# Performance work log

Hardware: AMD Instinct MI355X
Metric: run time of the kernel (lower is better)

Reference implementation:

```python
import jax, jax.numpy as jnp
import numpy as np

N_NODES = 100000
N_EDGES = 1600000
D_IN = 64


def _graph_conv(x, edge_src, edge_dst, W, b, n_nodes):
    # gather source features along edges, mean-aggregate at destinations,
    # then linear transform + ReLU (standard GraphConv semantics)
    msgs = x[edge_src]  # [E, d]
    agg = jax.ops.segment_sum(msgs, edge_dst, num_segments=n_nodes)  # [N, d]
    deg = jax.ops.segment_sum(jnp.ones((edge_src.shape[0],), x.dtype), edge_dst,
                              num_segments=n_nodes)  # [N]
    agg = agg / jnp.maximum(deg, 1.0)[:, None]
    return jax.nn.relu(agg @ W + b)


def setup_inputs() -> dict:
    key = jax.random.key(0)
    ks = jax.random.split(key, 6)
    node_features = jax.random.normal(ks[0], (N_NODES, D_IN), dtype=jnp.float32)
    edge_src = jax.random.randint(ks[1], (N_EDGES,), 0, N_NODES)
    edge_dst = jax.random.randint(ks[2], (N_EDGES,), 0, N_NODES)
    W1 = jax.random.normal(ks[3], (D_IN, 64), dtype=jnp.float32) * (1.0 / np.sqrt(D_IN))
    b1 = jnp.zeros((64,), jnp.float32)
    W2 = jax.random.normal(ks[4], (64, 32), dtype=jnp.float32) * (1.0 / np.sqrt(64))
    b2 = jnp.zeros((32,), jnp.float32)
    Wd = jax.random.normal(ks[5], (1, 1), dtype=jnp.float32)
    bd = jnp.zeros((1,), jnp.float32)
    return {"node_features": node_features, "edge_src": edge_src, "edge_dst": edge_dst,
            "W1": W1, "b1": b1, "W2": W2, "b2": b2, "Wd": Wd, "bd": bd}


def reference(node_features, edge_src, edge_dst, W1, b1, W2, b2, Wd, bd):
    n_nodes = node_features.shape[0]
    x = _graph_conv(node_features, edge_src, edge_dst, W1, b1, n_nodes)  # [N, 64]
    x = _graph_conv(x, edge_src, edge_dst, W2, b2, n_nodes)              # [N, 32]
    x = jnp.mean(x, axis=1, keepdims=True)                               # [N, 1]
    return jax.nn.sigmoid(x @ Wd + bd)                                   # [N, 1]
```

## Files before the change

### kernel.cpp

```cpp
#include <hip/hip_runtime.h>
#include <hip/hip_bf16.h>

#define N_NODES 100000
#define N_EDGES 1600000
#define N_PAD   100096
#define BSHIFT  10
#define NBUCKET 98
#define BCAP    19456
#define EPB     4096
#define NSCAT   391
#define NGEMM1  1563
#define PCAP    34816
#define ZROW    N_NODES

typedef float f32x2 __attribute__((ext_vector_type(2)));

__device__ __forceinline__ unsigned short f32_to_bf16(float f) {
    unsigned int u = __float_as_uint(f);
    unsigned int r = (u + 0x7fffu + ((u >> 16) & 1u)) >> 16;
    return (unsigned short)r;
}
__device__ __forceinline__ f32x2 up2(unsigned int p) {
    f32x2 r;
    r.x = __uint_as_float(p << 16);
    r.y = __uint_as_float(p & 0xffff0000u);
    return r;
}

__global__ void __launch_bounds__(256) k1_scatter_gemm64(
    const int* __restrict__ src, const int* __restrict__ dst,
    int* __restrict__ bcur, unsigned int* __restrict__ tmp,
    const float4* __restrict__ X4, const float* __restrict__ W,
    unsigned short* __restrict__ Y, int n_edges, int M) {
    extern __shared__ char smem[];
    int t = threadIdx.x;
    if (blockIdx.x < NSCAT) {
        int* lh = (int*)smem;
        int e0 = blockIdx.x * EPB;
        int ecnt = min(EPB, n_edges - e0);
        if (t < 128) lh[t] = 0;
        __syncthreads();
        const int4* s4 = (const int4*)(src + e0);
        const int4* d4 = (const int4*)(dst + e0);
        int4 sv[4], dv[4];
        #pragma unroll
        for (int j = 0; j < 4; j++) {
            int ib = t + j * 256;
            if (ib * 4 < ecnt) {
                sv[j] = s4[ib];
                dv[j] = d4[ib];
                atomicAdd(&lh[dv[j].x >> BSHIFT], 1);
                atomicAdd(&lh[dv[j].y >> BSHIFT], 1);
                atomicAdd(&lh[dv[j].z >> BSHIFT], 1);
                atomicAdd(&lh[dv[j].w >> BSHIFT], 1);
            }
        }
        __syncthreads();
        if (t < NBUCKET) {
            int c = lh[t];
            lh[t] = (c > 0) ? atomicAdd(&bcur[t], c) : 0;
        }
        __syncthreads();
        #pragma unroll
        for (int j = 0; j < 4; j++) {
            int ib = t + j * 256;
            if (ib * 4 < ecnt) {
                int ss[4] = {sv[j].x, sv[j].y, sv[j].z, sv[j].w};
                int dd[4] = {dv[j].x, dv[j].y, dv[j].z, dv[j].w};
                #pragma unroll
                for (int q = 0; q < 4; q++) {
                    int b = dd[q] >> BSHIFT;
                    int p = atomicAdd(&lh[b], 1);
                    if (p < BCAP)
                        tmp[(size_t)b * BCAP + p] =
                            ((unsigned)ss[q] << BSHIFT) | (unsigned)(dd[q] & 1023);
                }
            }
        }
        return;
    }
    float* sx = (float*)smem;
    float* sw = sx + 64 * 64;
    int base = (blockIdx.x - NSCAT) * 64;
    for (int i = t; i < 64 * 16; i += 256) {
        int r = i >> 4, c4 = i & 15;
        int row = base + r;
        float4 v = make_float4(0.f, 0.f, 0.f, 0.f);
        if (row < M) v = X4[(size_t)row * 16 + c4];
        int colp = (c4 * 4 + (r & 60)) & 63;
        *(float4*)&sx[r * 64 + colp] = v;
    }
    float4* sw4 = (float4*)sw;
    const float4* W4 = (const float4*)W;
    for (int i = t; i < 64 * 16; i += 256) sw4[i] = W4[i];
    __syncthreads();

    int tm = t & 15;
    int tn = t >> 4;
    int rbase = tm * 4;
    float acc[4][4] = {{0.f}};
    #pragma unroll 8
    for (int k = 0; k < 64; k++) {
        float4 b = sw4[k * 16 + tn];
        int kk = (k + rbase) & 63;
        float a0 = sx[(rbase + 0) * 64 + kk], a1 = sx[(rbase + 1) * 64 + kk];
        float a2 = sx[(rbase + 2) * 64 + kk], a3 = sx[(rbase + 3) * 64 + kk];
        acc[0][0] = fmaf(a0, b.x, acc[0][0]); acc[0][1] = fmaf(a0, b.y, acc[0][1]);
        acc[0][2] = fmaf(a0, b.z, acc[0][2]); acc[0][3] = fmaf(a0, b.w, acc[0][3]);
        acc[1][0] = fmaf(a1, b.x, acc[1][0]); acc[1][1] = fmaf(a1, b.y, acc[1][1]);
        acc[1][2] = fmaf(a1, b.z, acc[1][2]); acc[1][3] = fmaf(a1, b.w, acc[1][3]);
        acc[2][0] = fmaf(a2, b.x, acc[2][0]); acc[2][1] = fmaf(a2, b.y, acc[2][1]);
        acc[2][2] = fmaf(a2, b.z, acc[2][2]); acc[2][3] = fmaf(a2, b.w, acc[2][3]);
        acc[3][0] = fmaf(a3, b.x, acc[3][0]); acc[3][1] = fmaf(a3, b.y, acc[3][1]);
        acc[3][2] = fmaf(a3, b.z, acc[3][2]); acc[3][3] = fmaf(a3, b.w, acc[3][3]);
    }
    #pragma unroll
    for (int i = 0; i < 4; i++) {
        int row = base + rbase + i;
        if (row <= M) {
            ushort4 p;
            p.x = f32_to_bf16(acc[i][0]); p.y = f32_to_bf16(acc[i][1]);
            p.z = f32_to_bf16(acc[i][2]); p.w = f32_to_bf16(acc[i][3]);
            *(ushort4*)&Y[(size_t)row * 64 + tn * 4] = p;
        }
    }
}

__global__ void __launch_bounds__(1024) bucket_to_csr(
    const unsigned int* __restrict__ tmp, const int* __restrict__ bcur,
    int2* __restrict__ meta, int* __restrict__ col, int n_nodes) {
    __shared__ int nh[1024];
    __shared__ int wsum[16];
    int b = blockIdx.x;
    int t = threadIdx.x;
    int m = min(bcur[b], BCAP);
    const unsigned int* te = tmp + (size_t)b * BCAP;
    nh[t] = 0;
    __syncthreads();
    unsigned int rc[16];
    #pragma unroll
    for (int j = 0; j < 16; j++) {
        int i = t + j * 1024;
        if (i < m) {
            rc[j] = te[i];
            atomicAdd(&nh[rc[j] & 1023], 1);
        }
    }
    for (int i = t + 16384; i < m; i += 1024)
        atomicAdd(&nh[te[i] & 1023], 1);
    __syncthreads();
    int d  = nh[t];
    int pc = (d + 31) & ~31;
    int lane = t & 63;
    int incl = pc;
    #pragma unroll
    for (int o = 1; o < 64; o <<= 1) {
        int u = __shfl_up(incl, o);
        if (lane >= o) incl += u;
    }
    int w = t >> 6;
    if (lane == 63) wsum[w] = incl;
    __syncthreads();
    int woff = 0;
    #pragma unroll
    for (int q = 0; q < 16; q++) woff += (q < w) ? wsum[q] : 0;
    int begin = b * PCAP + woff + incl - pc;
    int node = (b << BSHIFT) + t;
    if (node < n_nodes) meta[node] = make_int2(begin, d);
    uint4 zz = make_uint4(ZROW, ZROW, ZROW, ZROW);
    uint4* cp = (uint4*)(col + begin);
    for (int q = 0; q < (pc >> 2); q++) cp[q] = zz;
    nh[t] = begin;
    __syncthreads();
    #pragma unroll
    for (int j = 0; j < 16; j++) {
        int i = t + j * 1024;
        if (i < m) {
            unsigned int e = rc[j];
            int pos = atomicAdd(&nh[e & 1023], 1);
            col[pos] = (int)(e >> BSHIFT);
        }
    }
    for (int i = t + 16384; i < m; i += 1024) {
        unsigned int e = te[i];
        int pos = atomicAdd(&nh[e & 1023], 1);
        col[pos] = (int)(e >> BSHIFT);
    }
}

__global__ void __launch_bounds__(256) gemm_n32(const float4* __restrict__ X4,
                                                const float* __restrict__ W,
                                                unsigned short* __restrict__ Z, int M) {
    __shared__ float sx[128][65];
    __shared__ float sw[64 * 32];
    int t = threadIdx.x;
    int base = blockIdx.x * 128;
    for (int i = t; i < 128 * 16; i += 256) {
        int r = i >> 4, c4 = i & 15;
        int row = base + r;
        float4 v = make_float4(0.f, 0.f, 0.f, 0.f);
        if (row < M) v = X4[(size_t)row * 16 + c4];
        sx[r][c4 * 4 + 0] = v.x; sx[r][c4 * 4 + 1] = v.y;
        sx[r][c4 * 4 + 2] = v.z; sx[r][c4 * 4 + 3] = v.w;
    }
    float4* sw4 = (float4*)sw;
    const float4* W4 = (const float4*)W;
    for (int i = t; i < 64 * 8; i += 256) sw4[i] = W4[i];
    __syncthreads();

    int tm = t & 31;
    int tn = t >> 5;
    float acc[4][4] = {{0.f}};
    #pragma unroll 8
    for (int k = 0; k < 64; k++) {
        float4 b = sw4[k * 8 + tn];
        float a0 = sx[tm * 4 + 0][k], a1 = sx[tm * 4 + 1][k];
        float a2 = sx[tm * 4 + 2][k], a3 = sx[tm * 4 + 3][k];
        acc[0][0] = fmaf(a0, b.x, acc[0][0]); acc[0][1] = fmaf(a0, b.y, acc[0][1]);
        acc[0][2] = fmaf(a0, b.z, acc[0][2]); acc[0][3] = fmaf(a0, b.w, acc[0][3]);
        acc[1][0] = fmaf(a1, b.x, acc[1][0]); acc[1][1] = fmaf(a1, b.y, acc[1][1]);
        acc[1][2] = fmaf(a1, b.z, acc[1][2]); acc[1][3] = fmaf(a1, b.w, acc[1][3]);
        acc[2][0] = fmaf(a2, b.x, acc[2][0]); acc[2][1] = fmaf(a2, b.y, acc[2][1]);
        acc[2][2] = fmaf(a2, b.z, acc[2][2]); acc[2][3] = fmaf(a2, b.w, acc[2][3]);
        acc[3][0] = fmaf(a3, b.x, acc[3][0]); acc[3][1] = fmaf(a3, b.y, acc[3][1]);
        acc[3][2] = fmaf(a3, b.z, acc[3][2]); acc[3][3] = fmaf(a3, b.w, acc[3][3]);
    }
    #pragma unroll
    for (int i = 0; i < 4; i++) {
        int row = base + tm * 4 + i;
        if (row <= M) {
            ushort4 p;
            p.x = f32_to_bf16(acc[i][0]); p.y = f32_to_bf16(acc[i][1]);
            p.z = f32_to_bf16(acc[i][2]); p.w = f32_to_bf16(acc[i][3]);
            *(ushort4*)&Z[(size_t)row * 32 + tn * 4] = p;
        }
    }
}

__global__ void __launch_bounds__(256) gather_relu64(
    const uint4* __restrict__ Y4, const int2* __restrict__ meta,
    const int* __restrict__ col, const float* __restrict__ b1,
    float4* __restrict__ H4, int n_nodes) {
    int n = blockIdx.x * 4 + (threadIdx.x >> 6);
    if (n >= n_nodes) return;
    int lane = threadIdx.x & 63;
    int g = lane >> 3;
    int c = lane & 7;
    int2 md = meta[n];
    int beg = md.x;
    int d = md.y;

    f32x2 acc[4];
    acc[0] = 0.f; acc[1] = 0.f; acc[2] = 0.f; acc[3] = 0.f;
    for (int i = 0; i < d; i += 32) {
        int s0 = col[beg + i + g];
        int s1 = col[beg + i + g + 8];
        int s2 = col[beg + i + g + 16];
        int s3 = col[beg + i + g + 24];
        uint4 v0 = Y4[(size_t)s0 * 8 + c];
        uint4 v1 = Y4[(size_t)s1 * 8 + c];
        uint4 v2 = Y4[(size_t)s2 * 8 + c];
        uint4 v3 = Y4[(size_t)s3 * 8 + c];
        acc[0] += (up2(v0.x) + up2(v1.x)) + (up2(v2.x) + up2(v3.x));
        acc[1] += (up2(v0.y) + up2(v1.y)) + (up2(v2.y) + up2(v3.y));
        acc[2] += (up2(v0.z) + up2(v1.z)) + (up2(v2.z) + up2(v3.z));
        acc[3] += (up2(v0.w) + up2(v1.w)) + (up2(v2.w) + up2(v3.w));
    }
    #pragma unroll
    for (int m = 8; m <= 32; m <<= 1) {
        #pragma unroll
        for (int q = 0; q < 4; q++) {
            acc[q].x += __shfl_xor(acc[q].x, m);
            acc[q].y += __shfl_xor(acc[q].y, m);
        }
    }
    float inv = 1.0f / fmaxf((float)d, 1.0f);
    const float4* b1_4 = (const float4*)b1;
    float4 ba = b1_4[c * 2], bb = b1_4[c * 2 + 1];
    if (g == 0) {
        float4 o0, o1;
        o0.x = fmaxf(fmaf(acc[0].x, inv, ba.x), 0.f);
        o0.y = fmaxf(fmaf(acc[0].y, inv, ba.y), 0.f);
        o0.z = fmaxf(fmaf(acc[1].x, inv, ba.z), 0.f);
        o0.w = fmaxf(fmaf(acc[1].y, inv, ba.w), 0.f);
        o1.x = fmaxf(fmaf(acc[2].x, inv, bb.x), 0.f);
        o1.y = fmaxf(fmaf(acc[2].y, inv, bb.y), 0.f);
        o1.z = fmaxf(fmaf(acc[3].x, inv, bb.z), 0.f);
        o1.w = fmaxf(fmaf(acc[3].y, inv, bb.w), 0.f);
        H4[(size_t)n * 16 + c * 2]     = o0;
        H4[(size_t)n * 16 + c * 2 + 1] = o1;
    }
}

__global__ void __launch_bounds__(256) gather_final32(
    const uint2* __restrict__ Z2, const int2* __restrict__ meta,
    const int* __restrict__ col, const float* __restrict__ b2,
    const float* __restrict__ Wd, const float* __restrict__ bd,
    float* __restrict__ out, int n_nodes) {
    int n = blockIdx.x * 4 + (threadIdx.x >> 6);
    if (n >= n_nodes) return;
    int lane = threadIdx.x & 63;
    int g = lane >> 3;
    int c = lane & 7;
    int2 md = meta[n];
    int beg = md.x;
    int d = md.y;

    f32x2 a01 = 0.f, a23 = 0.f;
    for (int i = 0; i < d; i += 32) {
        int s0 = col[beg + i + g];
        int s1 = col[beg + i + g + 8];
        int s2 = col[beg + i + g + 16];
        int s3 = col[beg + i + g + 24];
        uint2 v0 = Z2[(size_t)s0 * 8 + c];
        uint2 v1 = Z2[(size_t)s1 * 8 + c];
        uint2 v2 = Z2[(size_t)s2 * 8 + c];
        uint2 v3 = Z2[(size_t)s3 * 8 + c];
        a01 += (up2(v0.x) + up2(v1.x)) + (up2(v2.x) + up2(v3.x));
        a23 += (up2(v0.y) + up2(v1.y)) + (up2(v2.y) + up2(v3.y));
    }
    #pragma unroll
    for (int m = 8; m <= 32; m <<= 1) {
        a01.x += __shfl_xor(a01.x, m);
        a01.y += __shfl_xor(a01.y, m);
        a23.x += __shfl_xor(a23.x, m);
        a23.y += __shfl_xor(a23.y, m);
    }
    float inv = 1.0f / fmaxf((float)d, 1.0f);
    const float4* b2_4 = (const float4*)b2;
    float4 ba = b2_4[c];
    float local = fmaxf(fmaf(a01.x, inv, ba.x), 0.f)
                + fmaxf(fmaf(a01.y, inv, ba.y), 0.f)
                + fmaxf(fmaf(a23.x, inv, ba.z), 0.f)
                + fmaxf(fmaf(a23.y, inv, ba.w), 0.f);
    local += __shfl_xor(local, 1);
    local += __shfl_xor(local, 2);
    local += __shfl_xor(local, 4);
    if (lane == 0) {
        float z = fmaf(local * (1.0f / 32.0f), Wd[0], bd[0]);
        out[n] = 1.0f / (1.0f + __expf(-z));
    }
}

extern "C" void kernel_launch(void* const* d_in, const int* in_sizes, int n_in,
                              void* d_out, int out_size, void* d_ws, size_t ws_size,
                              hipStream_t stream) {
    const float* x    = (const float*)d_in[0];
    const int*   esrc = (const int*)d_in[1];
    const int*   edst = (const int*)d_in[2];
    const float* W1   = (const float*)d_in[3];
    const float* b1   = (const float*)d_in[4];
    const float* W2   = (const float*)d_in[5];
    const float* b2   = (const float*)d_in[6];
    const float* Wd   = (const float*)d_in[7];
    const float* bd   = (const float*)d_in[8];
    float* out = (float*)d_out;

    int*  bcur = (int*)d_ws;
    int2* meta = (int2*)(bcur + 128);
    int*  col  = (int*)(meta + N_PAD);
    float* h   = (float*)(col + (size_t)NBUCKET * PCAP + 1024);
    unsigned int* tmp = (unsigned int*)h;
    unsigned short* y  = (unsigned short*)(h + (size_t)N_NODES * 64);
    unsigned short* z2 = y + (size_t)(N_NODES + 1) * 64;

    hipMemsetAsync((void*)bcur, 0, 128 * sizeof(int), stream);

    k1_scatter_gemm64<<<NSCAT + NGEMM1, 256, 32768, stream>>>(
        esrc, edst, bcur, tmp, (const float4*)x, W1, y, N_EDGES, N_NODES);
    bucket_to_csr<<<NBUCKET, 1024, 0, stream>>>(tmp, bcur, meta, col, N_NODES);
    gather_relu64<<<(N_NODES + 3) / 4, 256, 0, stream>>>(
        (const uint4*)y, meta, col, b1, (float4*)h, N_NODES);
    gemm_n32<<<(N_NODES + 127) / 128, 256, 0, stream>>>((const float4*)h, W2, z2, N_NODES);
    gather_final32<<<(N_NODES + 3) / 4, 256, 0, stream>>>(
        (const uint2*)z2, meta, col, b2, Wd, bd, out, N_NODES);
}
```

Baseline: 238.9 us.

## Fuse GNN pipeline into one cooperative persistent kernel with grid syncs

Replaces the five separate launches (plus memset) with a single cooperative persistent kernel that runs every stage in grid-stride loops separated by grid.sync(). It also changes bucketing to 256-node buckets (391 buckets) and shrinks the GEMM tiles to 32/64 rows per block. The aim is to remove launch gaps and the memset. The cost is grid-wide barriers, occupancy limited to the co-resident grid, and smaller per-block tiles in the GEMMs. The old kernels are kept as a fallback if the cooperative launch fails.

```diff
diff --git a/kernel.cpp b/kernel.cpp
--- a/kernel.cpp
+++ b/kernel.cpp
@@ -1,9 +1,25 @@
 #include <hip/hip_runtime.h>
+#include <hip/hip_cooperative_groups.h>
 #include <hip/hip_bf16.h>
+
+namespace cg = cooperative_groups;
 
 #define N_NODES 100000
 #define N_EDGES 1600000
 #define N_PAD   100096
+#define ZROW    N_NODES
+
+#define MBSHIFT  8
+#define MNBUCKET 391
+#define MBCAP    4608
+#define MEPB     4096
+#define MNSCAT   391
+#define MNG64    3126
+#define MNG32    1563
+#define MNGATH   25000
+#define MPCAP    12544
+#define SMEMB    24832
+
 #define BSHIFT  10
 #define NBUCKET 98
 #define BCAP    19456
@@ -11,7 +27,6 @@
 #define NSCAT   391
 #define NGEMM1  1563
 #define PCAP    34816
-#define ZROW    N_NODES
 
 typedef float f32x2 __attribute__((ext_vector_type(2)));
 
@@ -27,15 +42,307 @@
     return r;
 }
 
+__global__ void __launch_bounds__(256) gnn_mega(
+    const int* __restrict__ esrc, const int* __restrict__ edst,
+    int* __restrict__ bcur, unsigned int* __restrict__ tmp,
+    const float4* __restrict__ X4, const float* __restrict__ W1,
+    unsigned short* __restrict__ Y, int2* __restrict__ meta,
+    int* __restrict__ col, const float* __restrict__ b1,
+    float* __restrict__ H, const float* __restrict__ W2,
+    unsigned short* __restrict__ Z, const float* __restrict__ b2,
+    const float* __restrict__ Wd, const float* __restrict__ bd,
+    float* __restrict__ out) {
+    __shared__ __align__(16) char smem[SMEMB];
+    cg::grid_group grid = cg::this_grid();
+    const int t = threadIdx.x;
+    const int G = gridDim.x;
+
+    if (blockIdx.x == 0) { for (int i = t; i < 512; i += 256) bcur[i] = 0; }
+    grid.sync();
+
+    for (int vb = blockIdx.x; vb < MNSCAT + MNG64; vb += G) {
+        __syncthreads();
+        if (vb < MNSCAT) {
+            int* lh = (int*)smem;
+            int e0 = vb * MEPB;
+            int ecnt = min(MEPB, N_EDGES - e0);
+            for (int i = t; i < 512; i += 256) lh[i] = 0;
+            __syncthreads();
+            const int4* s4 = (const int4*)(esrc + e0);
+            const int4* d4 = (const int4*)(edst + e0);
+            int4 sv[4], dv[4];
+            #pragma unroll
+            for (int j = 0; j < 4; j++) {
+                int ib = t + j * 256;
+                if (ib * 4 < ecnt) {
+                    sv[j] = s4[ib]; dv[j] = d4[ib];
+                    atomicAdd(&lh[dv[j].x >> MBSHIFT], 1);
+                    atomicAdd(&lh[dv[j].y >> MBSHIFT], 1);
+                    atomicAdd(&lh[dv[j].z >> MBSHIFT], 1);
+                    atomicAdd(&lh[dv[j].w >> MBSHIFT], 1);
+                }
+            }
+            __syncthreads();
+            for (int i = t; i < MNBUCKET; i += 256) {
+                int c = lh[i];
+                lh[i] = (c > 0) ? atomicAdd(&bcur[i], c) : 0;
+            }
+            __syncthreads();
+            #pragma unroll
+            for (int j = 0; j < 4; j++) {
+                int ib = t + j * 256;
+                if (ib * 4 < ecnt) {
+                    int ss[4] = {sv[j].x, sv[j].y, sv[j].z, sv[j].w};
+                    int dd[4] = {dv[j].x, dv[j].y, dv[j].z, dv[j].w};
+                    #pragma unroll
+                    for (int q = 0; q < 4; q++) {
+                        int b = dd[q] >> MBSHIFT;
+                        int p = atomicAdd(&lh[b], 1);
+                        if (p < MBCAP)
+                            tmp[(size_t)b * MBCAP + p] =
+                                ((unsigned)ss[q] << MBSHIFT) | (unsigned)(dd[q] & 255);
+                    }
+                }
+            }
+        } else {
+            int base = (vb - MNSCAT) * 32;
+            float* sx = (float*)smem;
+            float* sw = sx + 32 * 65;
+            for (int i = t; i < 32 * 16; i += 256) {
+                int r = i >> 4, c4 = i & 15;
+                int row = base + r;
+                float4 v = make_float4(0.f, 0.f, 0.f, 0.f);
+                if (row < N_NODES) v = X4[(size_t)row * 16 + c4];
+                sx[r * 65 + c4 * 4 + 0] = v.x; sx[r * 65 + c4 * 4 + 1] = v.y;
+                sx[r * 65 + c4 * 4 + 2] = v.z; sx[r * 65 + c4 * 4 + 3] = v.w;
+            }
+            float4* sw4 = (float4*)sw;
+            const float4* W4 = (const float4*)W1;
+            for (int i = t; i < 1024; i += 256) sw4[i] = W4[i];
+            __syncthreads();
+            int tm = t & 15;
+            int tn = t >> 4;
+            float acc[2][4] = {{0.f}};
+            #pragma unroll 8
+            for (int k = 0; k < 64; k++) {
+                float4 b = sw4[k * 16 + tn];
+                float a0 = sx[(2 * tm + 0) * 65 + k];
+                float a1 = sx[(2 * tm + 1) * 65 + k];
+                acc[0][0]=fmaf(a0,b.x,acc[0][0]); acc[0][1]=fmaf(a0,b.y,acc[0][1]);
+                acc[0][2]=fmaf(a0,b.z,acc[0][2]); acc[0][3]=fmaf(a0,b.w,acc[0][3]);
+                acc[1][0]=fmaf(a1,b.x,acc[1][0]); acc[1][1]=fmaf(a1,b.y,acc[1][1]);
+                acc[1][2]=fmaf(a1,b.z,acc[1][2]); acc[1][3]=fmaf(a1,b.w,acc[1][3]);
+            }
+            #pragma unroll
+            for (int i = 0; i < 2; i++) {
+                int row = base + 2 * tm + i;
+                if (row <= N_NODES) {
+                    ushort4 p;
+                    p.x = f32_to_bf16(acc[i][0]); p.y = f32_to_bf16(acc[i][1]);
+                    p.z = f32_to_bf16(acc[i][2]); p.w = f32_to_bf16(acc[i][3]);
+                    *(ushort4*)&Y[(size_t)row * 64 + tn * 4] = p;
+                }
+            }
+        }
+    }
+    grid.sync();
+
+    for (int vb = blockIdx.x; vb < MNBUCKET; vb += G) {
+        __syncthreads();
+        int* nh   = (int*)smem;
+        int* wsum = nh + 256;
+        int m = min(bcur[vb], MBCAP);
+        const unsigned int* te = tmp + (size_t)vb * MBCAP;
+        nh[t] = 0;
+        __syncthreads();
+        for (int i = t; i < m; i += 256) atomicAdd(&nh[te[i] & 255], 1);
+        __syncthreads();
+        int d  = nh[t];
+        int pc = (d + 31) & ~31;
+        int lane = t & 63;
+        int incl = pc;
+        #pragma unroll
+        for (int o = 1; o < 64; o <<= 1) {
+            int u = __shfl_up(incl, o);
+            if (lane >= o) incl += u;
+        }
+        int w = t >> 6;
+        if (lane == 63) wsum[w] = incl;
+        __syncthreads();
+        int woff = 0;
+        #pragma unroll
+        for (int q = 0; q < 4; q++) woff += (q < w) ? wsum[q] : 0;
+        int begin = vb * MPCAP + woff + incl - pc;
+        int node = (vb << MBSHIFT) + t;
+        if (node < N_NODES) meta[node] = make_int2(begin, d);
+        uint4 zz = make_uint4(ZROW, ZROW, ZROW, ZROW);
+        uint4* cp = (uint4*)(col + begin);
+        for (int q = 0; q < (pc >> 2); q++) cp[q] = zz;
+        __syncthreads();
+        nh[t] = begin;
+        __syncthreads();
+        for (int i = t; i < m; i += 256) {
+            unsigned int e = te[i];
+            int pos = atomicAdd(&nh[e & 255], 1);
+            col[pos] = (int)(e >> MBSHIFT);
+        }
+    }
+    grid.sync();
+
+    {
+        int lane = t & 63;
+        int g = lane >> 3, c = lane & 7;
+        const uint4* Y4 = (const uint4*)Y;
+        float4* H4 = (float4*)H;
+        const float4* b1_4 = (const float4*)b1;
+        float4 ba = b1_4[c * 2], bb = b1_4[c * 2 + 1];
+        for (int vb = blockIdx.x; vb < MNGATH; vb += G) {
+            int n = vb * 4 + (t >> 6);
+            if (n >= N_NODES) continue;
+            int2 md = meta[n];
+            int beg = md.x, d = md.y;
+            f32x2 acc[4];
+            acc[0] = 0.f; acc[1] = 0.f; acc[2] = 0.f; acc[3] = 0.f;
+            for (int i = 0; i < d; i += 32) {
+                int s0 = col[beg + i + g];
+                int s1 = col[beg + i + g + 8];
+                int s2 = col[beg + i + g + 16];
+                int s3 = col[beg + i + g + 24];
+                uint4 v0 = Y4[(size_t)s0 * 8 + c];
+                uint4 v1 = Y4[(size_t)s1 * 8 + c];
+                uint4 v2 = Y4[(size_t)s2 * 8 + c];
+                uint4 v3 = Y4[(size_t)s3 * 8 + c];
+                acc[0] += (up2(v0.x) + up2(v1.x)) + (up2(v2.x) + up2(v3.x));
+                acc[1] += (up2(v0.y) + up2(v1.y)) + (up2(v2.y) + up2(v3.y));
+                acc[2] += (up2(v0.z) + up2(v1.z)) + (up2(v2.z) + up2(v3.z));
+                acc[3] += (up2(v0.w) + up2(v1.w)) + (up2(v2.w) + up2(v3.w));
+            }
+            #pragma unroll
+            for (int mm = 8; mm <= 32; mm <<= 1) {
+                #pragma unroll
+                for (int q = 0; q < 4; q++) {
+                    acc[q].x += __shfl_xor(acc[q].x, mm);
+                    acc[q].y += __shfl_xor(acc[q].y, mm);
+                }
+            }
+            float inv = 1.0f / fmaxf((float)d, 1.0f);
+            if (g == 0) {
+                float4 o0, o1;
+                o0.x = fmaxf(fmaf(acc[0].x, inv, ba.x), 0.f);
+                o0.y = fmaxf(fmaf(acc[0].y, inv, ba.y), 0.f);
+                o0.z = fmaxf(fmaf(acc[1].x, inv, ba.z), 0.f);
+                o0.w = fmaxf(fmaf(acc[1].y, inv, ba.w), 0.f);
+                o1.x = fmaxf(fmaf(acc[2].x, inv, bb.x), 0.f);
+                o1.y = fmaxf(fmaf(acc[2].y, inv, bb.y), 0.f);
+                o1.z = fmaxf(fmaf(acc[3].x, inv, bb.z), 0.f);
+                o1.w = fmaxf(fmaf(acc[3].y, inv, bb.w), 0.f);
+                H4[(size_t)n * 16 + c * 2]     = o0;
+                H4[(size_t)n * 16 + c * 2 + 1] = o1;
+            }
+        }
+    }
+    grid.sync();
+
+    for (int vb = blockIdx.x; vb < MNG32; vb += G) {
+        __syncthreads();
+        int base = vb * 64;
+        float* sx = (float*)smem;
+        float* sw = sx + 64 * 65;
+        const float4* H4 = (const float4*)H;
+        for (int i = t; i < 64 * 16; i += 256) {
+            int r = i >> 4, c4 = i & 15;
+            int row = base + r;
+            float4 v = make_float4(0.f, 0.f, 0.f, 0.f);
+            if (row < N_NODES) v = H4[(size_t)row * 16 + c4];
+            sx[r * 65 + c4 * 4 + 0] = v.x; sx[r * 65 + c4 * 4 + 1] = v.y;
+            sx[r * 65 + c4 * 4 + 2] = v.z; sx[r * 65 + c4 * 4 + 3] = v.w;
+        }
+        float4* sw4 = (float4*)sw;
+        const float4* W4 = (const float4*)W2;
+        for (int i = t; i < 512; i += 256) sw4[i] = W4[i];
+        __syncthreads();
+        int tm = t & 31;
+        int tn = t >> 5;
+        float acc[2][4] = {{0.f}};
+        #pragma unroll 8
+        for (int k = 0; k < 64; k++) {
+            float4 b = sw4[k * 8 + tn];
+            float a0 = sx[(2 * tm + 0) * 65 + k];
+            float a1 = sx[(2 * tm + 1) * 65 + k];
+            acc[0][0]=fmaf(a0,b.x,acc[0][0]); acc[0][1]=fmaf(a0,b.y,acc[0][1]);
+            acc[0][2]=fmaf(a0,b.z,acc[0][2]); acc[0][3]=fmaf(a0,b.w,acc[0][3]);
+            acc[1][0]=fmaf(a1,b.x,acc[1][0]); acc[1][1]=fmaf(a1,b.y,acc[1][1]);
+            acc[1][2]=fmaf(a1,b.z,acc[1][2]); acc[1][3]=fmaf(a1,b.w,acc[1][3]);
+        }
+        #pragma unroll
+        for (int i = 0; i < 2; i++) {
+            int row = base + 2 * tm + i;
+            if (row <= N_NODES) {
+                ushort4 p;
+                p.x = f32_to_bf16(acc[i][0]); p.y = f32_to_bf16(acc[i][1]);
+                p.z = f32_to_bf16(acc[i][2]); p.w = f32_to_bf16(acc[i][3]);
+                *(ushort4*)&Z[(size_t)row * 32 + tn * 4] = p;
+            }
+        }
+    }
+    grid.sync();
+
+    {
+        int lane = t & 63;
+        int g = lane >> 3, c = lane & 7;
+        const uint2* Z2 = (const uint2*)Z;
+        const float4* b2_4 = (const float4*)b2;
+        float4 ba = b2_4[c];
+        for (int vb = blockIdx.x; vb < MNGATH; vb += G) {
+            int n = vb * 4 + (t >> 6);
+            if (n >= N_NODES) continue;
+            int2 md = meta[n];
+            int beg = md.x, d = md.y;
+            f32x2 a01 = 0.f, a23 = 0.f;
+            for (int i = 0; i < d; i += 32) {
+                int s0 = col[beg + i + g];
+                int s1 = col[beg + i + g + 8];
+                int s2 = col[beg + i + g + 16];
+                int s3 = col[beg + i + g + 24];
+                uint2 v0 = Z2[(size_t)s0 * 8 + c];
+                uint2 v1 = Z2[(size_t)s1 * 8 + c];
+                uint2 v2 = Z2[(size_t)s2 * 8 + c];
+                uint2 v3 = Z2[(size_t)s3 * 8 + c];
+                a01 += (up2(v0.x) + up2(v1.x)) + (up2(v2.x) + up2(v3.x));
+                a23 += (up2(v0.y) + up2(v1.y)) + (up2(v2.y) + up2(v3.y));
+            }
+            #pragma unroll
+            for (int mm = 8; mm <= 32; mm <<= 1) {
+                a01.x += __shfl_xor(a01.x, mm);
+                a01.y += __shfl_xor(a01.y, mm);
+                a23.x += __shfl_xor(a23.x, mm);
+                a23.y += __shfl_xor(a23.y, mm);
+            }
+            float inv = 1.0f / fmaxf((float)d, 1.0f);
+            float local = fmaxf(fmaf(a01.x, inv, ba.x), 0.f)
+                        + fmaxf(fmaf(a01.y, inv, ba.y), 0.f)
+                        + fmaxf(fmaf(a23.x, inv, ba.z), 0.f)
+                        + fmaxf(fmaf(a23.y, inv, ba.w), 0.f);
+            local += __shfl_xor(local, 1);
+            local += __shfl_xor(local, 2);
+            local += __shfl_xor(local, 4);
+            if (lane == 0) {
+                float z = fmaf(local * (1.0f / 32.0f), Wd[0], bd[0]);
+                out[n] = 1.0f / (1.0f + __expf(-z));
+            }
+        }
+    }
+}
+
 __global__ void __launch_bounds__(256) k1_scatter_gemm64(
     const int* __restrict__ src, const int* __restrict__ dst,
     int* __restrict__ bcur, unsigned int* __restrict__ tmp,
     const float4* __restrict__ X4, const float* __restrict__ W,
     unsigned short* __restrict__ Y, int n_edges, int M) {
-    extern __shared__ char smem[];
+    extern __shared__ char smemd[];
     int t = threadIdx.x;
     if (blockIdx.x < NSCAT) {
-        int* lh = (int*)smem;
+        int* lh = (int*)smemd;
         int e0 = blockIdx.x * EPB;
         int ecnt = min(EPB, n_edges - e0);
         if (t < 128) lh[t] = 0;
@@ -47,8 +354,7 @@
         for (int j = 0; j < 4; j++) {
             int ib = t + j * 256;
             if (ib * 4 < ecnt) {
-                sv[j] = s4[ib];
-                dv[j] = d4[ib];
+                sv[j] = s4[ib]; dv[j] = d4[ib];
                 atomicAdd(&lh[dv[j].x >> BSHIFT], 1);
                 atomicAdd(&lh[dv[j].y >> BSHIFT], 1);
                 atomicAdd(&lh[dv[j].z >> BSHIFT], 1);
@@ -79,7 +385,7 @@
         }
         return;
     }
-    float* sx = (float*)smem;
+    float* sx = (float*)smemd;
     float* sw = sx + 64 * 64;
     int base = (blockIdx.x - NSCAT) * 64;
     for (int i = t; i < 64 * 16; i += 256) {
@@ -94,7 +400,6 @@
     const float4* W4 = (const float4*)W;
     for (int i = t; i < 64 * 16; i += 256) sw4[i] = W4[i];
     __syncthreads();
-
     int tm = t & 15;
     int tn = t >> 4;
     int rbase = tm * 4;
@@ -105,14 +410,14 @@
         int kk = (k + rbase) & 63;
         float a0 = sx[(rbase + 0) * 64 + kk], a1 = sx[(rbase + 1) * 64 + kk];
         float a2 = sx[(rbase + 2) * 64 + kk], a3 = sx[(rbase + 3) * 64 + kk];
-        acc[0][0] = fmaf(a0, b.x, acc[0][0]); acc[0][1] = fmaf(a0, b.y, acc[0][1]);
-        acc[0][2] = fmaf(a0, b.z, acc[0][2]); acc[0][3] = fmaf(a0, b.w, acc[0][3]);
-        acc[1][0] = fmaf(a1, b.x, acc[1][0]); acc[1][1] = fmaf(a1, b.y, acc[1][1]);
-        acc[1][2] = fmaf(a1, b.z, acc[1][2]); acc[1][3] = fmaf(a1, b.w, acc[1][3]);
-        acc[2][0] = fmaf(a2, b.x, acc[2][0]); acc[2][1] = fmaf(a2, b.y, acc[2][1]);
-        acc[2][2] = fmaf(a2, b.z, acc[2][2]); acc[2][3] = fmaf(a2, b.w, acc[2][3]);
-        acc[3][0] = fmaf(a3, b.x, acc[3][0]); acc[3][1] = fmaf(a3, b.y, acc[3][1]);
-        acc[3][2] = fmaf(a3, b.z, acc[3][2]); acc[3][3] = fmaf(a3, b.w, acc[3][3]);
+        acc[0][0]=fmaf(a0,b.x,acc[0][0]); acc[0][1]=fmaf(a0,b.y,acc[0][1]);
+        acc[0][2]=fmaf(a0,b.z,acc[0][2]); acc[0][3]=fmaf(a0,b.w,acc[0][3]);
+        acc[1][0]=fmaf(a1,b.x,acc[1][0]); acc[1][1]=fmaf(a1,b.y,acc[1][1]);
+        acc[1][2]=fmaf(a1,b.z,acc[1][2]); acc[1][3]=fmaf(a1,b.w,acc[1][3]);
+        acc[2][0]=fmaf(a2,b.x,acc[2][0]); acc[2][1]=fmaf(a2,b.y,acc[2][1]);
+        acc[2][2]=fmaf(a2,b.z,acc[2][2]); acc[2][3]=fmaf(a2,b.w,acc[2][3]);
+        acc[3][0]=fmaf(a3,b.x,acc[3][0]); acc[3][1]=fmaf(a3,b.y,acc[3][1]);
+        acc[3][2]=fmaf(a3,b.z,acc[3][2]); acc[3][3]=fmaf(a3,b.w,acc[3][3]);
     }
     #pragma unroll
     for (int i = 0; i < 4; i++) {
@@ -141,13 +446,9 @@
     #pragma unroll
     for (int j = 0; j < 16; j++) {
         int i = t + j * 1024;
-        if (i < m) {
-            rc[j] = te[i];
-            atomicAdd(&nh[rc[j] & 1023], 1);
-        }
-    }
-    for (int i = t + 16384; i < m; i += 1024)
-        atomicAdd(&nh[te[i] & 1023], 1);
+        if (i < m) { rc[j] = te[i]; atomicAdd(&nh[rc[j] & 1023], 1); }
+    }
+    for (int i = t + 16384; i < m; i += 1024) atomicAdd(&nh[te[i] & 1023], 1);
     __syncthreads();
     int d  = nh[t];
     int pc = (d + 31) & ~31;
@@ -207,7 +508,6 @@
     const float4* W4 = (const float4*)W;
     for (int i = t; i < 64 * 8; i += 256) sw4[i] = W4[i];
     __syncthreads();
-
     int tm = t & 31;
     int tn = t >> 5;
     float acc[4][4] = {{0.f}};
@@ -216,14 +516,14 @@
         float4 b = sw4[k * 8 + tn];
         float a0 = sx[tm * 4 + 0][k], a1 = sx[tm * 4 + 1][k];
         float a2 = sx[tm * 4 + 2][k], a3 = sx[tm * 4 + 3][k];
-        acc[0][0] = fmaf(a0, b.x, acc[0][0]); acc[0][1] = fmaf(a0, b.y, acc[0][1]);
-        acc[0][2] = fmaf(a0, b.z, acc[0][2]); acc[0][3] = fmaf(a0, b.w, acc[0][3]);
-        acc[1][0] = fmaf(a1, b.x, acc[1][0]); acc[1][1] = fmaf(a1, b.y, acc[1][1]);
-        acc[1][2] = fmaf(a1, b.z, acc[1][2]); acc[1][3] = fmaf(a1, b.w, acc[1][3]);
-        acc[2][0] = fmaf(a2, b.x, acc[2][0]); acc[2][1] = fmaf(a2, b.y, acc[2][1]);
-        acc[2][2] = fmaf(a2, b.z, acc[2][2]); acc[2][3] = fmaf(a2, b.w, acc[2][3]);
-        acc[3][0] = fmaf(a3, b.x, acc[3][0]); acc[3][1] = fmaf(a3, b.y, acc[3][1]);
-        acc[3][2] = fmaf(a3, b.z, acc[3][2]); acc[3][3] = fmaf(a3, b.w, acc[3][3]);
+        acc[0][0]=fmaf(a0,b.x,acc[0][0]); acc[0][1]=fmaf(a0,b.y,acc[0][1]);
+        acc[0][2]=fmaf(a0,b.z,acc[0][2]); acc[0][3]=fmaf(a0,b.w,acc[0][3]);
+        acc[1][0]=fmaf(a1,b.x,acc[1][0]); acc[1][1]=fmaf(a1,b.y,acc[1][1]);
+        acc[1][2]=fmaf(a1,b.z,acc[1][2]); acc[1][3]=fmaf(a1,b.w,acc[1][3]);
+        acc[2][0]=fmaf(a2,b.x,acc[2][0]); acc[2][1]=fmaf(a2,b.y,acc[2][1]);
+        acc[2][2]=fmaf(a2,b.z,acc[2][2]); acc[2][3]=fmaf(a2,b.w,acc[2][3]);
+        acc[3][0]=fmaf(a3,b.x,acc[3][0]); acc[3][1]=fmaf(a3,b.y,acc[3][1]);
+        acc[3][2]=fmaf(a3,b.z,acc[3][2]); acc[3][3]=fmaf(a3,b.w,acc[3][3]);
     }
     #pragma unroll
     for (int i = 0; i < 4; i++) {
@@ -249,7 +549,6 @@
     int2 md = meta[n];
     int beg = md.x;
     int d = md.y;
-
     f32x2 acc[4];
     acc[0] = 0.f; acc[1] = 0.f; acc[2] = 0.f; acc[3] = 0.f;
     for (int i = 0; i < d; i += 32) {
@@ -305,7 +604,6 @@
     int2 md = meta[n];
     int beg = md.x;
     int d = md.y;
-
     f32x2 a01 = 0.f, a23 = 0.f;
     for (int i = 0; i < d; i += 32) {
         int s0 = col[beg + i + g];
@@ -345,7 +643,7 @@
 extern "C" void kernel_launch(void* const* d_in, const int* in_sizes, int n_in,
                               void* d_out, int out_size, void* d_ws, size_t ws_size,
                               hipStream_t stream) {
-    const float* x    = (const float*)d_in[0];
+    const float4* x4  = (const float4*)d_in[0];
     const int*   esrc = (const int*)d_in[1];
     const int*   edst = (const int*)d_in[2];
     const float* W1   = (const float*)d_in[3];
@@ -357,21 +655,54 @@
     float* out = (float*)d_out;
 
     int*  bcur = (int*)d_ws;
-    int2* meta = (int2*)(bcur + 128);
+    int2* meta = (int2*)(bcur + 512);
     int*  col  = (int*)(meta + N_PAD);
-    float* h   = (float*)(col + (size_t)NBUCKET * PCAP + 1024);
+    float* h   = (float*)(col + (size_t)MNBUCKET * MPCAP + 64);
     unsigned int* tmp = (unsigned int*)h;
     unsigned short* y  = (unsigned short*)(h + (size_t)N_NODES * 64);
     unsigned short* z2 = y + (size_t)(N_NODES + 1) * 64;
 
-    hipMemsetAsync((void*)bcur, 0, 128 * sizeof(int), stream);
-
-    k1_scatter_gemm64<<<NSCAT + NGEMM1, 256, 32768, stream>>>(
-        esrc, edst, bcur, tmp, (const float4*)x, W1, y, N_EDGES, N_NODES);
-    bucket_to_csr<<<NBUCKET, 1024, 0, stream>>>(tmp, bcur, meta, col, N_NODES);
-    gather_relu64<<<(N_NODES + 3) / 4, 256, 0, stream>>>(
-        (const uint4*)y, meta, col, b1, (float4*)h, N_NODES);
-    gemm_n32<<<(N_NODES + 127) / 128, 256, 0, stream>>>((const float4*)h, W2, z2, N_NODES);
-    gather_final32<<<(N_NODES + 3) / 4, 256, 0, stream>>>(
-        (const uint2*)z2, meta, col, b2, Wd, bd, out, N_NODES);
-}
+    static int s_grid = 0;
+    if (s_grid == 0) {
+        int nb = 0;
+        if (hipOccupancyMaxActiveBlocksPerMultiprocessor(
+                &nb, (const void*)gnn_mega, 256, 0) != hipSuccess || nb < 1)
+            nb = 4;
+        s_grid = nb * 256;
+    }
+
+    void* args[17];
+    args[0]  = (void*)&esrc; args[1]  = (void*)&edst;
+    args[2]  = (void*)&bcur; args[3]  = (void*)&tmp;
+    args[4]  = (void*)&x4;   args[5]  = (void*)&W1;
+    args[6]  = (void*)&y;    args[7]  = (void*)&meta;
+    args[8]  = (void*)&col;  args[9]  = (void*)&b1;
+    args[10] = (void*)&h;    args[11] = (void*)&W2;
+    args[12] = (void*)&z2;   args[13] = (void*)&b2;
+    args[14] = (void*)&Wd;   args[15] = (void*)&bd;
+    args[16] = (void*)&out;
+
+    hipError_t err = hipLaunchCooperativeKernel(
+        (void*)gnn_mega, dim3(s_grid), dim3(256), args, 0, stream);
+
+    if (err != hipSuccess) {
+        int*  fbcur = (int*)d_ws;
+        int2* fmeta = (int2*)(fbcur + 128);
+        int*  fcol  = (int*)(fmeta + N_PAD);
+        float* fh   = (float*)(fcol + (size_t)NBUCKET * PCAP + 1024);
+        unsigned int* ftmp = (unsigned int*)fh;
+        unsigned short* fy  = (unsigned short*)(fh + (size_t)N_NODES * 64);
+        unsigned short* fz2 = fy + (size_t)(N_NODES + 1) * 64;
+
+        hipMemsetAsync((void*)fbcur, 0, 128 * sizeof(int), stream);
+        k1_scatter_gemm64<<<NSCAT + NGEMM1, 256, 32768, stream>>>(
+            esrc, edst, fbcur, ftmp, x4, W1, fy, N_EDGES, N_NODES);
+        bucket_to_csr<<<NBUCKET, 1024, 0, stream>>>(ftmp, fbcur, fmeta, fcol, N_NODES);
+        gather_relu64<<<(N_NODES + 3) / 4, 256, 0, stream>>>(
+            (const uint4*)fy, fmeta, fcol, b1, (float4*)fh, N_NODES);
+        gemm_n32<<<(N_NODES + 127) / 128, 256, 0, stream>>>(
+            (const float4*)fh, W2, fz2, N_NODES);
+        gather_final32<<<(N_NODES + 3) / 4, 256, 0, stream>>>(
+            (const uint2*)fz2, fmeta, fcol, b2, Wd, bd, out, N_NODES);
+    }
+}
```

Result: slower. 618.6 us (+158.9%).
